# Kernel optimization log

Measured on AMD Instinct MI355X. Metric: run time of the kernel, lower is better.

## Reference

```python
import jax, jax.numpy as jnp
import numpy as np

NUM_TOKENS = 16384
HIDDEN = 2048
NUM_EXPERTS = 64
TOP_K = 2


def setup_inputs() -> dict:
    key = jax.random.key(0)
    kx, kw = jax.random.split(key)
    x = jax.random.normal(kx, (NUM_TOKENS, HIDDEN), dtype=jnp.float32)
    # nn.Linear weight is (num_experts, hidden); store transposed for x @ W
    W_gate = jax.random.normal(kw, (HIDDEN, NUM_EXPERTS), dtype=jnp.float32) * (1.0 / np.sqrt(HIDDEN))
    return {"x": x, "W_gate": W_gate}


def reference(x, W_gate):
    # gate matmul + softmax over experts
    logits = jnp.einsum("th,he->te", x, W_gate)          # (T, E)
    probs = jax.nn.softmax(logits, axis=-1)
    # top-k selection and renormalization
    top_k_weights, top_k_indices = jax.lax.top_k(probs, TOP_K)  # (T, k), (T, k)
    top_k_weights = top_k_weights / (jnp.sum(top_k_weights, axis=-1, keepdims=True) + 1e-9)
    # Switch-style load-balancing aux loss using top-1 assignments
    num_tokens = x.shape[0]
    top1 = top_k_indices[:, 0]
    tokens_per_expert = jnp.zeros((NUM_EXPERTS,), dtype=probs.dtype).at[top1].add(1.0)
    f = tokens_per_expert / num_tokens                    # fraction of tokens per expert
    P = jnp.mean(probs, axis=0)                           # mean router prob per expert
    aux_loss = NUM_EXPERTS * jnp.sum(f * P)
    return (top_k_weights, top_k_indices, aux_loss)
```

## Files before the change

kernel.cpp:

```cpp
#include <hip/hip_runtime.h>
#include <math.h>

#define NUM_TOKENS 16384
#define HIDDEN 2048
#define NUM_EXPERTS 64

#define IDX_OFF 32768
#define AUX_OFF 65536

#define KSLICE 256

__global__ __launch_bounds__(512, 2) void router_kernel(
    const float* __restrict__ x, const float* __restrict__ Wg,
    float* __restrict__ out, float* __restrict__ ws)
{
    __shared__ float buf[4][64][68];
    __shared__ int top1s[64];

    const int tid  = threadIdx.x;
    const int w    = tid >> 6;
    const int lane = tid & 63;
    const int token = blockIdx.x * 64 + lane;

    const int k0 = __builtin_amdgcn_readfirstlane(w) * KSLICE;

    float C[64];
    #pragma unroll
    for (int e = 0; e < 64; ++e) C[e] = 0.f;

    const float4* xr = reinterpret_cast<const float4*>(x + (size_t)token * HIDDEN + k0);

    float4 cur = xr[0];
    for (int c = 0; c < KSLICE / 4; ++c) {
        float4 nxt = xr[(c + 1) & (KSLICE / 4 - 1)];
        const float xv[4] = {cur.x, cur.y, cur.z, cur.w};
        #pragma unroll
        for (int q = 0; q < 4; ++q) {
            const int k = k0 + c * 4 + q;
            const float* __restrict__ wrow = Wg + (size_t)k * NUM_EXPERTS;
            #pragma unroll
            for (int e = 0; e < 64; ++e)
                C[e] = fmaf(xv[q], wrow[e], C[e]);
        }
        cur = nxt;
    }

    #define WBUF(b) { _Pragma("unroll") for (int e4 = 0; e4 < 16; ++e4) { \
        float4 v; v.x = C[e4*4+0]; v.y = C[e4*4+1]; v.z = C[e4*4+2]; v.w = C[e4*4+3]; \
        *reinterpret_cast<float4*>(&buf[b][lane][e4*4]) = v; } }
    #define ABUF(b) { _Pragma("unroll") for (int e4 = 0; e4 < 16; ++e4) { \
        const float4 v = *reinterpret_cast<const float4*>(&buf[b][lane][e4*4]); \
        C[e4*4+0] += v.x; C[e4*4+1] += v.y; C[e4*4+2] += v.z; C[e4*4+3] += v.w; } }

    if (w >= 4) WBUF(w - 4);
    __syncthreads();
    if (w < 4) ABUF(w);
    __syncthreads();
    if (w == 2 || w == 3) WBUF(w - 2);
    __syncthreads();
    if (w < 2) ABUF(w);
    __syncthreads();
    if (w == 1) WBUF(0);
    __syncthreads();

    if (w == 0) {
        ABUF(0);

        float m = C[0];
        #pragma unroll
        for (int e = 1; e < 64; ++e) m = fmaxf(m, C[e]);
        float Z = 0.f;
        #pragma unroll
        for (int e = 0; e < 64; ++e) { C[e] = expf(C[e] - m); Z += C[e]; }
        const float rz = 1.f / Z;

        float v1 = -1.f, v2 = -1.f; int i1 = 0, i2 = 0;
        #pragma unroll
        for (int e = 0; e < 64; ++e) {
            const float p = C[e] * rz;
            C[e] = p;
            if (p > v1)      { v2 = v1; i2 = i1; v1 = p; i1 = e; }
            else if (p > v2) { v2 = p;  i2 = e; }
        }

        const float s = v1 + v2 + 1e-9f;
        float2 wo; wo.x = v1 / s; wo.y = v2 / s;
        *reinterpret_cast<float2*>(&out[(size_t)token * 2]) = wo;
        float2 io; io.x = (float)i1; io.y = (float)i2;
        *reinterpret_cast<float2*>(&out[IDX_OFF + (size_t)token * 2]) = io;

        WBUF(0);
        top1s[lane] = i1;
    }
    __syncthreads();

    if (w == 1) {
        float sp = 0.f;
        #pragma unroll 8
        for (int t = 0; t < 64; ++t) sp += buf[0][t][lane];
        float cnt = 0.f;
        #pragma unroll 8
        for (int t = 0; t < 64; ++t) cnt += (top1s[t] == lane) ? 1.f : 0.f;
        ws[(size_t)blockIdx.x * 128 + lane]      = sp;
        ws[(size_t)blockIdx.x * 128 + 64 + lane] = cnt;
    }
}

__global__ __launch_bounds__(64) void finalize_kernel(
    const float* __restrict__ ws, float* __restrict__ out)
{
    const int e = threadIdx.x;
    float sp = 0.f, sc = 0.f;
    for (int b = 0; b < NUM_TOKENS / 64; ++b) {
        sp += ws[(size_t)b * 128 + e];
        sc += ws[(size_t)b * 128 + 64 + e];
    }
    float val = (sc * (1.0f / NUM_TOKENS)) * (sp * (1.0f / NUM_TOKENS));
    #pragma unroll
    for (int off = 32; off >= 1; off >>= 1) val += __shfl_xor(val, off);
    if (e == 0) out[AUX_OFF] = (float)NUM_EXPERTS * val;
}

extern "C" void kernel_launch(void* const* d_in, const int* in_sizes, int n_in,
                              void* d_out, int out_size, void* d_ws, size_t ws_size,
                              hipStream_t stream) {
    const float* x  = (const float*)d_in[0];
    const float* Wg = (const float*)d_in[1];
    float* out = (float*)d_out;
    float* ws  = (float*)d_ws;

    router_kernel<<<NUM_TOKENS / 64, 512, 0, stream>>>(x, Wg, out, ws);
    finalize_kernel<<<1, 64, 0, stream>>>(ws, out);
}
```

Before: 104.6 us.

## Split router into split-K GEMM kernel with global partials and separate reduce kernel

```diff
diff --git a/kernel.cpp b/kernel.cpp
--- a/kernel.cpp
+++ b/kernel.cpp
@@ -8,21 +8,23 @@
 #define IDX_OFF 32768
 #define AUX_OFF 65536
 
-#define KSLICE 256
-
-__global__ __launch_bounds__(512, 2) void router_kernel(
+#define NSLICE 8
+#define KSL (HIDDEN / NSLICE)
+#define TB 512
+#define NTB (NUM_TOKENS / TB)
+#define PART_FLOATS ((size_t)NSLICE * NUM_TOKENS * NUM_EXPERTS)
+#define WS_NEEDED ((PART_FLOATS + (size_t)(NUM_TOKENS / 64) * 128) * sizeof(float))
+
+
+__global__ __launch_bounds__(512, 2) void gemm_kernel(
     const float* __restrict__ x, const float* __restrict__ Wg,
-    float* __restrict__ out, float* __restrict__ ws)
-{
-    __shared__ float buf[4][64][68];
-    __shared__ int top1s[64];
-
-    const int tid  = threadIdx.x;
-    const int w    = tid >> 6;
-    const int lane = tid & 63;
-    const int token = blockIdx.x * 64 + lane;
-
-    const int k0 = __builtin_amdgcn_readfirstlane(w) * KSLICE;
+    float* __restrict__ ws)
+{
+    const int tid = threadIdx.x;
+    const int tb  = blockIdx.x & (NTB - 1);
+    const int sl  = blockIdx.x >> 5;
+    const int token = tb * TB + tid;
+    const int k0 = sl * KSL;
 
     float C[64];
     #pragma unroll
@@ -31,8 +33,8 @@
     const float4* xr = reinterpret_cast<const float4*>(x + (size_t)token * HIDDEN + k0);
 
     float4 cur = xr[0];
-    for (int c = 0; c < KSLICE / 4; ++c) {
-        float4 nxt = xr[(c + 1) & (KSLICE / 4 - 1)];
+    for (int c = 0; c < KSL / 4; ++c) {
+        float4 nxt = xr[(c + 1) & (KSL / 4 - 1)];
         const float xv[4] = {cur.x, cur.y, cur.z, cur.w};
         #pragma unroll
         for (int q = 0; q < 4; ++q) {
@@ -45,6 +47,113 @@
         cur = nxt;
     }
 
+    float* pr = ws + ((size_t)sl * NUM_TOKENS + token) * NUM_EXPERTS;
+    #pragma unroll
+    for (int e4 = 0; e4 < 16; ++e4) {
+        float4 v; v.x = C[e4*4+0]; v.y = C[e4*4+1]; v.z = C[e4*4+2]; v.w = C[e4*4+3];
+        *reinterpret_cast<float4*>(pr + e4 * 4) = v;
+    }
+}
+
+__global__ __launch_bounds__(64) void reduce_kernel(
+    const float* __restrict__ ws, float* __restrict__ out, float* __restrict__ ws_aux)
+{
+    __shared__ float pbuf[64][68];
+    __shared__ int top1s[64];
+
+    const int lane = threadIdx.x;
+    const int token = blockIdx.x * 64 + lane;
+
+    float C[64];
+    #pragma unroll
+    for (int e = 0; e < 64; ++e) C[e] = 0.f;
+
+    for (int s = 0; s < NSLICE; ++s) {
+        const float* pr = ws + ((size_t)s * NUM_TOKENS + token) * NUM_EXPERTS;
+        #pragma unroll
+        for (int e4 = 0; e4 < 16; ++e4) {
+            const float4 v = *reinterpret_cast<const float4*>(pr + e4 * 4);
+            C[e4*4+0] += v.x; C[e4*4+1] += v.y; C[e4*4+2] += v.z; C[e4*4+3] += v.w;
+        }
+    }
+
+    float m = C[0];
+    #pragma unroll
+    for (int e = 1; e < 64; ++e) m = fmaxf(m, C[e]);
+    float Z = 0.f;
+    #pragma unroll
+    for (int e = 0; e < 64; ++e) { C[e] = expf(C[e] - m); Z += C[e]; }
+    const float rz = 1.f / Z;
+
+    float v1 = -1.f, v2 = -1.f; int i1 = 0, i2 = 0;
+    #pragma unroll
+    for (int e = 0; e < 64; ++e) {
+        const float p = C[e] * rz;
+        C[e] = p;
+        if (p > v1)      { v2 = v1; i2 = i1; v1 = p; i1 = e; }
+        else if (p > v2) { v2 = p;  i2 = e; }
+    }
+
+    const float s = v1 + v2 + 1e-9f;
+    float2 wo; wo.x = v1 / s; wo.y = v2 / s;
+    *reinterpret_cast<float2*>(&out[(size_t)token * 2]) = wo;
+    float2 io; io.x = (float)i1; io.y = (float)i2;
+    *reinterpret_cast<float2*>(&out[IDX_OFF + (size_t)token * 2]) = io;
+
+    #pragma unroll
+    for (int e4 = 0; e4 < 16; ++e4)
+        *reinterpret_cast<float4*>(&pbuf[lane][e4 * 4]) =
+            make_float4(C[e4*4+0], C[e4*4+1], C[e4*4+2], C[e4*4+3]);
+    top1s[lane] = i1;
+    __syncthreads();
+
+    float sp = 0.f;
+    #pragma unroll 8
+    for (int t = 0; t < 64; ++t) sp += pbuf[t][lane];
+    float cnt = 0.f;
+    #pragma unroll 8
+    for (int t = 0; t < 64; ++t) cnt += (top1s[t] == lane) ? 1.f : 0.f;
+    ws_aux[(size_t)blockIdx.x * 128 + lane]      = sp;
+    ws_aux[(size_t)blockIdx.x * 128 + 64 + lane] = cnt;
+}
+
+
+#define KSLICE 256
+
+__global__ __launch_bounds__(512, 2) void router_fallback(
+    const float* __restrict__ x, const float* __restrict__ Wg,
+    float* __restrict__ out, float* __restrict__ ws)
+{
+    __shared__ float buf[4][64][68];
+    __shared__ int top1s[64];
+
+    const int tid  = threadIdx.x;
+    const int w    = tid >> 6;
+    const int lane = tid & 63;
+    const int token = blockIdx.x * 64 + lane;
+    const int k0 = __builtin_amdgcn_readfirstlane(w) * KSLICE;
+
+    float C[64];
+    #pragma unroll
+    for (int e = 0; e < 64; ++e) C[e] = 0.f;
+
+    const float4* xr = reinterpret_cast<const float4*>(x + (size_t)token * HIDDEN + k0);
+
+    float4 cur = xr[0];
+    for (int c = 0; c < KSLICE / 4; ++c) {
+        float4 nxt = xr[(c + 1) & (KSLICE / 4 - 1)];
+        const float xv[4] = {cur.x, cur.y, cur.z, cur.w};
+        #pragma unroll
+        for (int q = 0; q < 4; ++q) {
+            const int k = k0 + c * 4 + q;
+            const float* __restrict__ wrow = Wg + (size_t)k * NUM_EXPERTS;
+            #pragma unroll
+            for (int e = 0; e < 64; ++e)
+                C[e] = fmaf(xv[q], wrow[e], C[e]);
+        }
+        cur = nxt;
+    }
+
     #define WBUF(b) { _Pragma("unroll") for (int e4 = 0; e4 < 16; ++e4) { \
         float4 v; v.x = C[e4*4+0]; v.y = C[e4*4+1]; v.z = C[e4*4+2]; v.w = C[e4*4+3]; \
         *reinterpret_cast<float4*>(&buf[b][lane][e4*4]) = v; } }
@@ -65,7 +174,6 @@
 
     if (w == 0) {
         ABUF(0);
-
         float m = C[0];
         #pragma unroll
         for (int e = 1; e < 64; ++e) m = fmaxf(m, C[e]);
@@ -82,13 +190,11 @@
             if (p > v1)      { v2 = v1; i2 = i1; v1 = p; i1 = e; }
             else if (p > v2) { v2 = p;  i2 = e; }
         }
-
         const float s = v1 + v2 + 1e-9f;
         float2 wo; wo.x = v1 / s; wo.y = v2 / s;
         *reinterpret_cast<float2*>(&out[(size_t)token * 2]) = wo;
         float2 io; io.x = (float)i1; io.y = (float)i2;
         *reinterpret_cast<float2*>(&out[IDX_OFF + (size_t)token * 2]) = io;
-
         WBUF(0);
         top1s[lane] = i1;
     }
@@ -107,13 +213,13 @@
 }
 
 __global__ __launch_bounds__(64) void finalize_kernel(
-    const float* __restrict__ ws, float* __restrict__ out)
+    const float* __restrict__ ws_aux, float* __restrict__ out)
 {
     const int e = threadIdx.x;
     float sp = 0.f, sc = 0.f;
     for (int b = 0; b < NUM_TOKENS / 64; ++b) {
-        sp += ws[(size_t)b * 128 + e];
-        sc += ws[(size_t)b * 128 + 64 + e];
+        sp += ws_aux[(size_t)b * 128 + e];
+        sc += ws_aux[(size_t)b * 128 + 64 + e];
     }
     float val = (sc * (1.0f / NUM_TOKENS)) * (sp * (1.0f / NUM_TOKENS));
     #pragma unroll
@@ -129,6 +235,13 @@
     float* out = (float*)d_out;
     float* ws  = (float*)d_ws;
 
-    router_kernel<<<NUM_TOKENS / 64, 512, 0, stream>>>(x, Wg, out, ws);
-    finalize_kernel<<<1, 64, 0, stream>>>(ws, out);
-}
+    if (ws_size >= WS_NEEDED) {
+        float* ws_aux = ws + PART_FLOATS;
+        gemm_kernel<<<NTB * NSLICE, 512, 0, stream>>>(x, Wg, ws);
+        reduce_kernel<<<NUM_TOKENS / 64, 64, 0, stream>>>(ws, out, ws_aux);
+        finalize_kernel<<<1, 64, 0, stream>>>(ws_aux, out);
+    } else {
+        router_fallback<<<NUM_TOKENS / 64, 512, 0, stream>>>(x, Wg, out, ws);
+        finalize_kernel<<<1, 64, 0, stream>>>(ws, out);
+    }
+}
```

Measured after the change: 113.4 us. +8.5%, slower.
